# Performance work log

Measured on AMD Instinct MI355X. Metric: run time of the kernel, lower is better.

The kernel has to match this reference:

```python
import jax, jax.numpy as jnp
import numpy as np

B, N, M, C1, C2 = 8, 8192, 2048, 64, 128
MLP = [128, 128]
EPS = 1e-5


def setup_inputs() -> dict:
    key = jax.random.key(0)
    ks = jax.random.split(key, 12)
    inp = {
        'low_theta': jax.random.normal(ks[0], (B, N), jnp.float32),
        'low_phi': jax.random.normal(ks[1], (B, N), jnp.float32),
        'low_feats': jax.random.normal(ks[2], (B, C1, N), jnp.float32),
        'high_theta': jax.random.normal(ks[3], (B, M), jnp.float32),
        'high_phi': jax.random.normal(ks[4], (B, M), jnp.float32),
        'high_feats': jax.random.normal(ks[5], (B, C2, M), jnp.float32),
    }
    in_ch = C1 + C2
    # layer 0: conv1d (kernel size 1) -> weight [out, in], bias [out]; BN gamma/beta
    inp['W0'] = jax.random.normal(ks[6], (MLP[0], in_ch), jnp.float32) * 0.05
    inp['b0'] = jnp.zeros((MLP[0],), jnp.float32)
    inp['g0'] = jnp.ones((MLP[0],), jnp.float32)
    inp['beta0'] = jnp.zeros((MLP[0],), jnp.float32)
    # layer 1
    inp['W1'] = jax.random.normal(ks[7], (MLP[1], MLP[0]), jnp.float32) * 0.05
    inp['b1'] = jnp.zeros((MLP[1],), jnp.float32)
    inp['g1'] = jnp.ones((MLP[1],), jnp.float32)
    inp['beta1'] = jnp.zeros((MLP[1],), jnp.float32)
    return inp


def _conv_bn_relu(x, W, b, gamma, beta):
    # x: [B, Cin, N] -> 1x1 conv -> BN (training-mode batch stats, biased var) -> ReLU
    y = jnp.einsum('oi,bin->bon', W, x) + b[None, :, None]
    mean = jnp.mean(y, axis=(0, 2), keepdims=True)
    var = jnp.mean((y - mean) ** 2, axis=(0, 2), keepdims=True)
    yhat = (y - mean) * jax.lax.rsqrt(var + EPS)
    return jax.nn.relu(gamma[None, :, None] * yhat + beta[None, :, None])


def reference(low_theta, low_phi, low_feats, high_theta, high_phi, high_feats,
              W0, b0, g0, beta0, W1, b1, g1, beta1):
    # pairwise angular distance [B, N, M]
    dtheta = low_theta[:, :, None] - high_theta[:, None, :]
    dphi = low_phi[:, :, None] - high_phi[:, None, :]
    dist = jnp.sqrt(dtheta ** 2 + dphi ** 2)
    idx = jnp.argmin(dist, axis=-1)  # [B, N]
    # gather nearest-neighbor high features -> [B, C2, N]
    c2 = high_feats.shape[1]
    interpolated = jnp.take_along_axis(
        high_feats, jnp.broadcast_to(idx[:, None, :], (idx.shape[0], c2, idx.shape[1])), axis=2)
    cat = jnp.concatenate([low_feats, interpolated], axis=1)  # [B, C1+C2, N]
    h = _conv_bn_relu(cat, W0, b0, g0, beta0)
    out = _conv_bn_relu(h, W1, b1, g1, beta1)
    return out
```

## Files before the change

### kernel.cpp

```cpp
#include <hip/hip_runtime.h>
#include <hip/hip_bf16.h>

#define BB 8
#define NN 8192
#define MM 2048
#define C1 64
#define C2 128
#define CIN 192
#define CO 128
#define NB (BB*NN)
#define EPS 1e-5f

#define PRE_ARGMIN 2048
#define PRE_PREPH  (PRE_ARGMIN + 512)
#define PRE_TOTAL  (PRE_PREPH + 96)

typedef unsigned short u16;
typedef unsigned int u32;
typedef __bf16 bf16_t;
typedef bf16_t bf16x8 __attribute__((ext_vector_type(8)));
typedef float f32x4 __attribute__((ext_vector_type(4)));
typedef float f32x2 __attribute__((ext_vector_type(2)));

static __device__ __forceinline__ float b2f(u16 u) { return __uint_as_float(((u32)u) << 16); }
static __device__ __forceinline__ u16 f2b(float f) {
    __hip_bfloat16 h = __float2bfloat16(f);
    u16 u; __builtin_memcpy(&u, &h, 2); return u;
}

__global__ __launch_bounds__(256) void k_pre(
        const float* __restrict__ lt_, const float* __restrict__ lp_,
        const float* __restrict__ ht_, const float* __restrict__ hp_,
        const float* __restrict__ hf, const float* __restrict__ W0, const float* __restrict__ W1,
        int* __restrict__ idx, u16* __restrict__ hT,
        u16* __restrict__ W0b, u16* __restrict__ W1b) {
    __shared__ float smem[2 * 8 * 260];
    int bid = blockIdx.x, tid = threadIdx.x;

    if (bid < PRE_ARGMIN) {
        int b = bid >> 8;
        int n0 = (bid & 255) << 5;
        float* nx = smem;
        float* ny = smem + 8 * 260;
        for (int e = tid; e < MM; e += 256) {
            int p = e >> 8, i = e & 255;
            nx[p * 260 + i] = -ht_[b * MM + e];
            ny[p * 260 + i] = -hp_[b * MM + e];
        }
        __syncthreads();
        int q = tid >> 3, p = tid & 7;
        float ltv = lt_[b * NN + n0 + q];
        float lpv = lp_[b * NN + n0 + q];
        f32x2 lt2 = {ltv, ltv}, lp2 = {lpv, lpv};
        float dl[4] = {1e30f, 1e30f, 1e30f, 1e30f};
        float dpv[4] = {1e30f, 1e30f, 1e30f, 1e30f};
        int il[4] = {0, 0, 0, 0}, ipx[4] = {0, 0, 0, 0};
        const float* nxp = &nx[p * 260];
        const float* nyp = &ny[p * 260];
#pragma unroll 4
        for (int k = 0; k < 32; ++k) {
#pragma unroll
            for (int c = 0; c < 4; ++c) {
                f32x2 xx = *(const f32x2*)&nxp[(k << 3) + (c << 1)];
                f32x2 yy = *(const f32x2*)&nyp[(k << 3) + (c << 1)];
                f32x2 dt, dq, t2, u2, d2;
                asm("v_pk_add_f32 %0, %1, %2" : "=v"(dt) : "v"(lt2), "v"(xx));
                asm("v_pk_add_f32 %0, %1, %2" : "=v"(dq) : "v"(lp2), "v"(yy));
                asm("v_pk_mul_f32 %0, %1, %2" : "=v"(t2) : "v"(dt), "v"(dt));
                asm("v_pk_mul_f32 %0, %1, %2" : "=v"(u2) : "v"(dq), "v"(dq));
                asm("v_pk_add_f32 %0, %1, %2" : "=v"(d2) : "v"(t2), "v"(u2));
                int i0 = (k << 3) + (c << 1);
                bool h0 = d2[0] < dl[c];
                dpv[c] = h0 ? dl[c] : dpv[c];
                ipx[c] = h0 ? il[c] : ipx[c];
                dl[c] = h0 ? d2[0] : dl[c];
                il[c] = h0 ? i0 : il[c];
                bool h1 = d2[1] < dl[c];
                dpv[c] = h1 ? dl[c] : dpv[c];
                ipx[c] = h1 ? il[c] : ipx[c];
                dl[c] = h1 ? d2[1] : dl[c];
                il[c] = h1 ? i0 + 1 : il[c];
            }
        }
        int mbase = p << 8;
        float bs = 1e30f; int bm = 0x7fffffff;
#pragma unroll
        for (int c = 0; c < 4; ++c) {
            float sl = __fsqrt_rn(dl[c]);
            float sp = __fsqrt_rn(dpv[c]);
            int cand = mbase + ((sp == sl) ? ipx[c] : il[c]);
            if (sl < bs || (sl == bs && cand < bm)) { bs = sl; bm = cand; }
        }
#pragma unroll
        for (int d = 1; d <= 4; d <<= 1) {
            float ov = __shfl_xor(bs, d, 64);
            int om = __shfl_xor(bm, d, 64);
            if (ov < bs || (ov == bs && om < bm)) { bs = ov; bm = om; }
        }
        if (p == 0) idx[b * NN + n0 + q] = bm;
    } else if (bid < PRE_PREPH) {
        u16 (*s)[65] = (u16(*)[65])smem;
        int bid2 = bid - PRE_ARGMIN;
        int b = bid2 >> 6, m0 = ((bid2 >> 1) & 31) * 64, c0 = (bid2 & 1) * 64;
        for (int e = tid; e < 64 * 64; e += 256) {
            int i = e >> 6, j = e & 63;
            s[i][j] = f2b(hf[(b * C2 + c0 + i) * MM + m0 + j]);
        }
        __syncthreads();
        for (int e = tid; e < 64 * 64; e += 256) {
            int ii = e & 63, jj = e >> 6;
            hT[(b * MM + m0 + jj) * C2 + c0 + ii] = s[ii][jj];
        }
    } else {
        int t = (bid - PRE_PREPH) * 256 + tid;
        if (t < CIN * CO) W0b[t] = f2b(W0[t]);
        if (t < CO * CO)  W1b[t] = f2b(W1[t]);
    }
}

static __device__ __forceinline__ void epilogue(
        f32x4* ac0, f32x4* ac1, const float* bias, u16* yl,
        float* chs, float* chq, int w, int ln, int q) {
#pragma unroll
    for (int mf = 0; mf < 2; ++mf) {
        f32x4* A = mf ? ac1 : ac0;
        int chb = 32 * w + 16 * mf + 4 * q;
        float bs[4], ss[4] = {0.f, 0.f, 0.f, 0.f}, sq[4] = {0.f, 0.f, 0.f, 0.f};
#pragma unroll
        for (int r = 0; r < 4; ++r) bs[r] = bias[chb + r];
#pragma unroll
        for (int nf = 0; nf < 4; ++nf) {
            int n = (nf << 4) + ln;
#pragma unroll
            for (int r = 0; r < 4; ++r) {
                float y = A[nf][r] + bs[r];
                ss[r] += y; sq[r] += y * y;
                int o = chb + r;
                yl[(o << 6) + (n ^ ((o & 7) << 3))] = f2b(y);
            }
        }
#pragma unroll
        for (int r = 0; r < 4; ++r) {
            float v = ss[r], u2 = sq[r];
#pragma unroll
            for (int d = 1; d < 16; d <<= 1) {
                v += __shfl_xor(v, d, 64);
                u2 += __shfl_xor(u2, d, 64);
            }
            if (ln == 0) { atomicAdd(&chs[chb + r], v); atomicAdd(&chq[chb + r], u2); }
        }
    }
}

__global__ __launch_bounds__(256) void k_l0(
        const float* __restrict__ lf, const u16* __restrict__ hT, const int* __restrict__ idx,
        const u16* __restrict__ W0b, const float* __restrict__ b0,
        u16* __restrict__ y0, float* __restrict__ gpart) {
    __shared__ u16 xt[64 * CIN];
    __shared__ u16 ylds[CO * 64];
    __shared__ float chs[CO], chq[CO];
    __shared__ int idxs[64];
    int tid = threadIdx.x;
    int l = tid & 63, w = tid >> 6, ln = l & 15, q = l >> 4;
    int b = blockIdx.x >> 7, n0 = (blockIdx.x & 127) << 6;
    if (tid < 64) idxs[tid] = idx[b * NN + n0 + tid];
    if (tid < 128) { chs[tid] = 0.f; chq[tid] = 0.f; }
    __syncthreads();
    {
        const float* src = lf + (size_t)(b * C1 + l) * NN + n0 + (w << 4);
        float4 f0 = *(const float4*)src;
        float4 f1 = *(const float4*)(src + 4);
        float4 f2 = *(const float4*)(src + 8);
        float4 f3 = *(const float4*)(src + 12);
        float v[16] = {f0.x, f0.y, f0.z, f0.w, f1.x, f1.y, f1.z, f1.w,
                       f2.x, f2.y, f2.z, f2.w, f3.x, f3.y, f3.z, f3.w};
        int cc = l >> 3, clo = l & 7;
#pragma unroll
        for (int i = 0; i < 16; ++i) {
            int n = (w << 4) + i;
            xt[n * CIN + ((cc ^ (i & 7)) << 3) + clo] = f2b(v[i]);
        }
    }
    for (int e = tid; e < 1024; e += 256) {
        int n = e >> 4, c16 = e & 15;
        uint4 v = *(const uint4*)(hT + (size_t)(b * MM + idxs[n]) * C2 + (c16 << 3));
        *(uint4*)&xt[n * CIN + (((8 + c16) ^ (n & 7)) << 3)] = v;
    }
    __syncthreads();
    f32x4 ac0[4], ac1[4];
#pragma unroll
    for (int nf = 0; nf < 4; ++nf) {
        ac0[nf] = f32x4{0.f, 0.f, 0.f, 0.f};
        ac1[nf] = f32x4{0.f, 0.f, 0.f, 0.f};
    }
    const u16* w0r0 = W0b + (32 * w + ln) * CIN + 8 * q;
    const u16* w0r1 = w0r0 + 16 * CIN;
#pragma unroll
    for (int s = 0; s < 6; ++s) {
        bf16x8 a0 = *(const bf16x8*)(w0r0 + 32 * s);
        bf16x8 a1 = *(const bf16x8*)(w0r1 + 32 * s);
#pragma unroll
        for (int nf = 0; nf < 4; ++nf) {
            bf16x8 bv = *(const bf16x8*)&xt[(16 * nf + ln) * CIN + (((4 * s + q) ^ (ln & 7)) << 3)];
            ac0[nf] = __builtin_amdgcn_mfma_f32_16x16x32_bf16(a0, bv, ac0[nf], 0, 0, 0);
            ac1[nf] = __builtin_amdgcn_mfma_f32_16x16x32_bf16(a1, bv, ac1[nf], 0, 0, 0);
        }
    }
    epilogue(ac0, ac1, b0, ylds, chs, chq, w, ln, q);
    __syncthreads();
    gpart[blockIdx.x * 256 + tid] = (tid < 128) ? chs[tid] : chq[tid - 128];
    {
        int o = tid >> 1, h = tid & 1;
#pragma unroll
        for (int jj = 0; jj < 4; ++jj) {
            int j = (h << 2) + jj;
            uint4 v = *(const uint4*)&ylds[(o << 6) + ((j ^ (o & 7)) << 3)];
            *(uint4*)(y0 + (size_t)(b * CO + o) * NN + n0 + (j << 3)) = v;
        }
    }
}

__global__ __launch_bounds__(256) void k_red_scale(
        const float* __restrict__ gpart, const float* __restrict__ g,
        const float* __restrict__ be, float* __restrict__ sc, float* __restrict__ sh) {
    __shared__ float wsum[4], wsq[4];
    int o = blockIdx.x, tid = threadIdx.x;
    float s = 0.f, q = 0.f;
#pragma unroll
    for (int j = 0; j < 4; ++j) {
        int k = tid + (j << 8);
        s += gpart[k * 256 + o];
        q += gpart[k * 256 + 128 + o];
    }
#pragma unroll
    for (int d = 1; d < 64; d <<= 1) {
        s += __shfl_xor(s, d, 64);
        q += __shfl_xor(q, d, 64);
    }
    if ((tid & 63) == 0) { wsum[tid >> 6] = s; wsq[tid >> 6] = q; }
    __syncthreads();
    if (tid == 0) {
        float st = (wsum[0] + wsum[1]) + (wsum[2] + wsum[3]);
        float qt = (wsq[0] + wsq[1]) + (wsq[2] + wsq[3]);
        float mu = st * (1.f / NB);
        float var = qt * (1.f / NB) - mu * mu;
        float istd = 1.f / __fsqrt_rn(var + EPS);
        float scale = g[o] * istd;
        sc[o] = scale;
        sh[o] = be[o] - mu * scale;
    }
}

__global__ __launch_bounds__(256) void k_l1(
        u16* __restrict__ y, const float* __restrict__ sc0, const float* __restrict__ sh0,
        const u16* __restrict__ W1b, const float* __restrict__ b1,
        float* __restrict__ gpart) {
    __shared__ u16 xt[64 * CO];
    __shared__ u16 ylds[CO * 64];
    __shared__ float chs[CO], chq[CO], sc[CO], sh[CO];
    int tid = threadIdx.x;
    int l = tid & 63, w = tid >> 6, ln = l & 15, q = l >> 4;
    int b = blockIdx.x >> 7, n0 = (blockIdx.x & 127) << 6;
    if (tid < 128) {
        sc[tid] = sc0[tid]; sh[tid] = sh0[tid];
        chs[tid] = 0.f; chq[tid] = 0.f;
    }
    __syncthreads();
#pragma unroll
    for (int it = 0; it < 2; ++it) {
        int c = (it << 6) + l;
        const u16* src = y + (size_t)(b * CO + c) * NN + n0 + (w << 4);
        uint4 r0 = *(const uint4*)src;
        uint4 r1 = *(const uint4*)(src + 8);
        u16 raw[16];
        *(uint4*)&raw[0] = r0;
        *(uint4*)&raw[8] = r1;
        float scale = sc[c], shift = sh[c];
        int cc = c >> 3, clo = c & 7;
#pragma unroll
        for (int i = 0; i < 16; ++i) {
            int n = (w << 4) + i;
            float hv = fmaxf(b2f(raw[i]) * scale + shift, 0.f);
            xt[(n << 7) + ((cc ^ (i & 7)) << 3) + clo] = f2b(hv);
        }
    }
    __syncthreads();
    f32x4 ac0[4], ac1[4];
#pragma unroll
    for (int nf = 0; nf < 4; ++nf) {
        ac0[nf] = f32x4{0.f, 0.f, 0.f, 0.f};
        ac1[nf] = f32x4{0.f, 0.f, 0.f, 0.f};
    }
    const u16* w1r0 = W1b + (32 * w + ln) * CO + 8 * q;
    const u16* w1r1 = w1r0 + 16 * CO;
#pragma unroll
    for (int s = 0; s < 4; ++s) {
        bf16x8 a0 = *(const bf16x8*)(w1r0 + 32 * s);
        bf16x8 a1 = *(const bf16x8*)(w1r1 + 32 * s);
#pragma unroll
        for (int nf = 0; nf < 4; ++nf) {
            bf16x8 bv = *(const bf16x8*)&xt[((16 * nf + ln) << 7) + (((4 * s + q) ^ (ln & 7)) << 3)];
            ac0[nf] = __builtin_amdgcn_mfma_f32_16x16x32_bf16(a0, bv, ac0[nf], 0, 0, 0);
            ac1[nf] = __builtin_amdgcn_mfma_f32_16x16x32_bf16(a1, bv, ac1[nf], 0, 0, 0);
        }
    }
    epilogue(ac0, ac1, b1, ylds, chs, chq, w, ln, q);
    __syncthreads();
    gpart[blockIdx.x * 256 + tid] = (tid < 128) ? chs[tid] : chq[tid - 128];
    {
        int o = tid >> 1, h = tid & 1;
#pragma unroll
        for (int jj = 0; jj < 4; ++jj) {
            int j = (h << 2) + jj;
            uint4 v = *(const uint4*)&ylds[(o << 6) + ((j ^ (o & 7)) << 3)];
            *(uint4*)(y + (size_t)(b * CO + o) * NN + n0 + (j << 3)) = v;
        }
    }
}

__global__ __launch_bounds__(256) void k_bn1(
        const u16* __restrict__ y, const float* __restrict__ gpart,
        const float* __restrict__ g1, const float* __restrict__ be1,
        float* __restrict__ out) {
    __shared__ float wsum[4], wsq[4], bcast[2];
    int tid = threadIdx.x, bid = blockIdx.x;
    int o = (bid >> 2) & 127;
    float s = 0.f, q = 0.f;
#pragma unroll
    for (int j = 0; j < 4; ++j) {
        int k = tid + (j << 8);
        s += gpart[k * 256 + o];
        q += gpart[k * 256 + 128 + o];
    }
#pragma unroll
    for (int d = 1; d < 64; d <<= 1) {
        s += __shfl_xor(s, d, 64);
        q += __shfl_xor(q, d, 64);
    }
    if ((tid & 63) == 0) { wsum[tid >> 6] = s; wsq[tid >> 6] = q; }
    __syncthreads();
    if (tid == 0) {
        float st = (wsum[0] + wsum[1]) + (wsum[2] + wsum[3]);
        float qt = (wsq[0] + wsq[1]) + (wsq[2] + wsq[3]);
        float mu = st * (1.f / NB);
        float var = qt * (1.f / NB) - mu * mu;
        float istd = 1.f / __fsqrt_rn(var + EPS);
        float scale = g1[o] * istd;
        bcast[0] = scale;
        bcast[1] = be1[o] - mu * scale;
    }
    __syncthreads();
    float scale = bcast[0], shift = bcast[1];
    int t = bid * 256 + tid;
    size_t e0 = (size_t)t << 3;
    uint4 v = *(const uint4*)(y + e0);
    u16 raw[8];
    *(uint4*)raw = v;
    float r[8];
#pragma unroll
    for (int k = 0; k < 8; ++k)
        r[k] = fmaxf(b2f(raw[k]) * scale + shift, 0.f);
    *(float4*)(out + e0) = make_float4(r[0], r[1], r[2], r[3]);
    *(float4*)(out + e0 + 4) = make_float4(r[4], r[5], r[6], r[7]);
}

extern "C" void kernel_launch(void* const* d_in, const int* in_sizes, int n_in,
                              void* d_out, int out_size, void* d_ws, size_t ws_size,
                              hipStream_t stream) {
    const float* lt = (const float*)d_in[0];
    const float* lp = (const float*)d_in[1];
    const float* lf = (const float*)d_in[2];
    const float* ht = (const float*)d_in[3];
    const float* hp = (const float*)d_in[4];
    const float* hf = (const float*)d_in[5];
    const float* W0 = (const float*)d_in[6];
    const float* b0 = (const float*)d_in[7];
    const float* g0 = (const float*)d_in[8];
    const float* be0 = (const float*)d_in[9];
    const float* W1 = (const float*)d_in[10];
    const float* b1 = (const float*)d_in[11];
    const float* g1 = (const float*)d_in[12];
    const float* be1 = (const float*)d_in[13];

    char* ws = (char*)d_ws;
    u16* y0 = (u16*)ws;
    u16* hT = (u16*)(ws + 16777216);
    int* idx = (int*)(ws + 20971520);
    float* sc0 = (float*)(ws + 21233664);
    float* sh0 = (float*)(ws + 21234176);
    u16* W0b = (u16*)(ws + 21235712);
    u16* W1b = (u16*)(ws + 21284864);
    float* gpart = (float*)(ws + 21317632);

    k_pre<<<PRE_TOTAL, 256, 0, stream>>>(lt, lp, ht, hp, hf, W0, W1,
                                         idx, hT, W0b, W1b);
    k_l0<<<1024, 256, 0, stream>>>(lf, hT, idx, W0b, b0, y0, gpart);
    k_red_scale<<<128, 256, 0, stream>>>(gpart, g0, be0, sc0, sh0);
    k_l1<<<1024, 256, 0, stream>>>(y0, sc0, sh0, W1b, b1, gpart);
    k_bn1<<<4096, 256, 0, stream>>>(y0, gpart, g1, be1, (float*)d_out);
}
```

Before: 120.3 us.

## Read high-res coordinates as scalar operands in argmin instead of LDS staging

Result: slower. 141.7 us (+17.8%).

```diff
diff --git a/kernel.cpp b/kernel.cpp
--- a/kernel.cpp
+++ b/kernel.cpp
@@ -11,7 +11,7 @@
 #define NB (BB*NN)
 #define EPS 1e-5f
 
-#define PRE_ARGMIN 2048
+#define PRE_ARGMIN 1024
 #define PRE_PREPH  (PRE_ARGMIN + 512)
 #define PRE_TOTAL  (PRE_PREPH + 96)
 
@@ -34,42 +34,38 @@
         const float* __restrict__ hf, const float* __restrict__ W0, const float* __restrict__ W1,
         int* __restrict__ idx, u16* __restrict__ hT,
         u16* __restrict__ W0b, u16* __restrict__ W1b) {
-    __shared__ float smem[2 * 8 * 260];
+    __shared__ u16 s_t[64][65];
+    __shared__ float sm_s[256];
+    __shared__ int sm_i[256];
     int bid = blockIdx.x, tid = threadIdx.x;
 
     if (bid < PRE_ARGMIN) {
-        int b = bid >> 8;
-        int n0 = (bid & 255) << 5;
-        float* nx = smem;
-        float* ny = smem + 8 * 260;
-        for (int e = tid; e < MM; e += 256) {
-            int p = e >> 8, i = e & 255;
-            nx[p * 260 + i] = -ht_[b * MM + e];
-            ny[p * 260 + i] = -hp_[b * MM + e];
-        }
-        __syncthreads();
-        int q = tid >> 3, p = tid & 7;
-        float ltv = lt_[b * NN + n0 + q];
-        float lpv = lp_[b * NN + n0 + q];
-        f32x2 lt2 = {ltv, ltv}, lp2 = {lpv, lpv};
+        int lane = tid & 63;
+        int b = bid >> 7;
+        int n0 = (bid & 127) << 6;
+        int w = __builtin_amdgcn_readfirstlane(tid >> 6);
+        int cbase = __builtin_amdgcn_readfirstlane(b * MM + (w << 9));
+        const float* hx = ht_ + cbase;
+        const float* hy = hp_ + cbase;
+        float ltv = lt_[b * NN + n0 + lane];
+        float lpv = lp_[b * NN + n0 + lane];
+        f32x2 nlt2 = {-ltv, -ltv}, nlp2 = {-lpv, -lpv};
         float dl[4] = {1e30f, 1e30f, 1e30f, 1e30f};
         float dpv[4] = {1e30f, 1e30f, 1e30f, 1e30f};
         int il[4] = {0, 0, 0, 0}, ipx[4] = {0, 0, 0, 0};
-        const float* nxp = &nx[p * 260];
-        const float* nyp = &ny[p * 260];
 #pragma unroll 4
-        for (int k = 0; k < 32; ++k) {
+        for (int k = 0; k < 64; ++k) {
 #pragma unroll
             for (int c = 0; c < 4; ++c) {
-                f32x2 xx = *(const f32x2*)&nxp[(k << 3) + (c << 1)];
-                f32x2 yy = *(const f32x2*)&nyp[(k << 3) + (c << 1)];
+                f32x2 xx = *(const f32x2*)&hx[(c << 7) + (k << 1)];
+                f32x2 yy = *(const f32x2*)&hy[(c << 7) + (k << 1)];
                 f32x2 dt, dq, t2, u2, d2;
-                asm("v_pk_add_f32 %0, %1, %2" : "=v"(dt) : "v"(lt2), "v"(xx));
-                asm("v_pk_add_f32 %0, %1, %2" : "=v"(dq) : "v"(lp2), "v"(yy));
+                asm("v_pk_add_f32 %0, %1, %2" : "=v"(dt) : "s"(xx), "v"(nlt2));
+                asm("v_pk_add_f32 %0, %1, %2" : "=v"(dq) : "s"(yy), "v"(nlp2));
                 asm("v_pk_mul_f32 %0, %1, %2" : "=v"(t2) : "v"(dt), "v"(dt));
                 asm("v_pk_mul_f32 %0, %1, %2" : "=v"(u2) : "v"(dq), "v"(dq));
                 asm("v_pk_add_f32 %0, %1, %2" : "=v"(d2) : "v"(t2), "v"(u2));
-                int i0 = (k << 3) + (c << 1);
+                int i0 = (w << 9) + (c << 7) + (k << 1);
                 bool h0 = d2[0] < dl[c];
                 dpv[c] = h0 ? dl[c] : dpv[c];
                 ipx[c] = h0 ? il[c] : ipx[c];
@@ -82,34 +78,38 @@
                 il[c] = h1 ? i0 + 1 : il[c];
             }
         }
-        int mbase = p << 8;
         float bs = 1e30f; int bm = 0x7fffffff;
 #pragma unroll
         for (int c = 0; c < 4; ++c) {
             float sl = __fsqrt_rn(dl[c]);
             float sp = __fsqrt_rn(dpv[c]);
-            int cand = mbase + ((sp == sl) ? ipx[c] : il[c]);
+            int cand = (sp == sl) ? ipx[c] : il[c];
             if (sl < bs || (sl == bs && cand < bm)) { bs = sl; bm = cand; }
         }
-#pragma unroll
-        for (int d = 1; d <= 4; d <<= 1) {
-            float ov = __shfl_xor(bs, d, 64);
-            int om = __shfl_xor(bm, d, 64);
-            if (ov < bs || (ov == bs && om < bm)) { bs = ov; bm = om; }
-        }
-        if (p == 0) idx[b * NN + n0 + q] = bm;
+        sm_s[(w << 6) + lane] = bs;
+        sm_i[(w << 6) + lane] = bm;
+        __syncthreads();
+        if (tid < 64) {
+            float fb = sm_s[tid]; int fm = sm_i[tid];
+#pragma unroll
+            for (int w2 = 1; w2 < 4; ++w2) {
+                float ov = sm_s[(w2 << 6) + tid];
+                int om = sm_i[(w2 << 6) + tid];
+                if (ov < fb || (ov == fb && om < fm)) { fb = ov; fm = om; }
+            }
+            idx[b * NN + n0 + tid] = fm;
+        }
     } else if (bid < PRE_PREPH) {
-        u16 (*s)[65] = (u16(*)[65])smem;
         int bid2 = bid - PRE_ARGMIN;
         int b = bid2 >> 6, m0 = ((bid2 >> 1) & 31) * 64, c0 = (bid2 & 1) * 64;
         for (int e = tid; e < 64 * 64; e += 256) {
             int i = e >> 6, j = e & 63;
-            s[i][j] = f2b(hf[(b * C2 + c0 + i) * MM + m0 + j]);
+            s_t[i][j] = f2b(hf[(b * C2 + c0 + i) * MM + m0 + j]);
         }
         __syncthreads();
         for (int e = tid; e < 64 * 64; e += 256) {
             int ii = e & 63, jj = e >> 6;
-            hT[(b * MM + m0 + jj) * C2 + c0 + ii] = s[ii][jj];
+            hT[(b * MM + m0 + jj) * C2 + c0 + ii] = s_t[ii][jj];
         }
     } else {
         int t = (bid - PRE_PREPH) * 256 + tid;
```

## Fuse all stages into one persistent cooperative kernel with on-chip intermediates

Applied to the files above, without the earlier changes.

New measurement: 120.3 us. About the same (-0.0%).

```diff
diff --git a/kernel.cpp b/kernel.cpp
--- a/kernel.cpp
+++ b/kernel.cpp
@@ -1,5 +1,8 @@
 #include <hip/hip_runtime.h>
 #include <hip/hip_bf16.h>
+#include <hip/hip_cooperative_groups.h>
+
+namespace cg = cooperative_groups;
 
 #define BB 8
 #define NN 8192
@@ -11,10 +14,6 @@
 #define NB (BB*NN)
 #define EPS 1e-5f
 
-#define PRE_ARGMIN 2048
-#define PRE_PREPH  (PRE_ARGMIN + 512)
-#define PRE_TOTAL  (PRE_PREPH + 96)
-
 typedef unsigned short u16;
 typedef unsigned int u32;
 typedef __bf16 bf16_t;
@@ -27,6 +26,327 @@
     __hip_bfloat16 h = __float2bfloat16(f);
     u16 u; __builtin_memcpy(&u, &h, 2); return u;
 }
+static __device__ __forceinline__ bf16x8 cvt8(float4 x, float4 y) {
+    union { u16 u[8]; bf16x8 v; } cv;
+    cv.u[0] = f2b(x.x); cv.u[1] = f2b(x.y); cv.u[2] = f2b(x.z); cv.u[3] = f2b(x.w);
+    cv.u[4] = f2b(y.x); cv.u[5] = f2b(y.y); cv.u[6] = f2b(y.z); cv.u[7] = f2b(y.w);
+    return cv.v;
+}
+
+static __device__ __forceinline__ void epilogue(
+        f32x4* ac0, f32x4* ac1, const float* bias, u16* yl,
+        float* chs, float* chq, int w, int ln, int q) {
+#pragma unroll
+    for (int mf = 0; mf < 2; ++mf) {
+        f32x4* A = mf ? ac1 : ac0;
+        int chb = 32 * w + 16 * mf + 4 * q;
+        float bs[4], ss[4] = {0.f, 0.f, 0.f, 0.f}, sq[4] = {0.f, 0.f, 0.f, 0.f};
+#pragma unroll
+        for (int r = 0; r < 4; ++r) bs[r] = bias[chb + r];
+#pragma unroll
+        for (int nf = 0; nf < 4; ++nf) {
+            int n = (nf << 4) + ln;
+#pragma unroll
+            for (int r = 0; r < 4; ++r) {
+                float y = A[nf][r] + bs[r];
+                ss[r] += y; sq[r] += y * y;
+                int o = chb + r;
+                yl[(o << 6) + (n ^ ((o & 7) << 3))] = f2b(y);
+            }
+        }
+#pragma unroll
+        for (int r = 0; r < 4; ++r) {
+            float v = ss[r], u2 = sq[r];
+#pragma unroll
+            for (int d = 1; d < 16; d <<= 1) {
+                v += __shfl_xor(v, d, 64);
+                u2 += __shfl_xor(u2, d, 64);
+            }
+            if (ln == 0) { atomicAdd(&chs[chb + r], v); atomicAdd(&chq[chb + r], u2); }
+        }
+    }
+}
+
+struct KArgs {
+    const float *lt, *lp, *ht, *hp, *hf, *lf;
+    const float *W0, *b0, *g0, *be0, *W1, *b1, *g1, *be1;
+    float* out;
+    u16* hT;
+    float *gpart, *sc0, *sh0, *sc1, *sh1;
+};
+
+__global__ __launch_bounds__(256, 2) void k_all(KArgs a) {
+    __shared__ unsigned long long scratch8[3104];
+    __shared__ u16 ylds[2][CO * 64];
+    __shared__ float chs[CO], chq[CO], scl[CO], shl[CO];
+    __shared__ int idxs[128];
+    __shared__ float wtmp[8];
+    cg::grid_group grid = cg::this_grid();
+    int bid = blockIdx.x, tid = threadIdx.x;
+    int b = bid >> 6, blk = bid & 63;
+    int l = tid & 63, w = tid >> 6, ln = l & 15, q = l >> 4;
+
+    {
+        float* nx = (float*)scratch8;
+        float* ny = nx + 8 * 260;
+        for (int e = tid; e < MM; e += 256) {
+            int p = e >> 8, i = e & 255;
+            nx[p * 260 + i] = -a.ht[b * MM + e];
+            ny[p * 260 + i] = -a.hp[b * MM + e];
+        }
+        __syncthreads();
+        int qq = tid >> 3, p = tid & 7;
+        const float* nxp = &nx[p * 260];
+        const float* nyp = &ny[p * 260];
+        int mbase = p << 8;
+        for (int r = 0; r < 4; ++r) {
+            int n0 = blk * 128 + r * 32;
+            float ltv = a.lt[b * NN + n0 + qq], lpv = a.lp[b * NN + n0 + qq];
+            f32x2 lt2 = {ltv, ltv}, lp2 = {lpv, lpv};
+            float dl[4] = {1e30f, 1e30f, 1e30f, 1e30f};
+            float dpv[4] = {1e30f, 1e30f, 1e30f, 1e30f};
+            int il[4] = {0, 0, 0, 0}, ipx[4] = {0, 0, 0, 0};
+#pragma unroll 4
+            for (int k = 0; k < 32; ++k) {
+#pragma unroll
+                for (int c = 0; c < 4; ++c) {
+                    f32x2 xx = *(const f32x2*)&nxp[(k << 3) + (c << 1)];
+                    f32x2 yy = *(const f32x2*)&nyp[(k << 3) + (c << 1)];
+                    f32x2 dt, dp2, t2, u2, d2;
+                    asm("v_pk_add_f32 %0, %1, %2" : "=v"(dt) : "v"(lt2), "v"(xx));
+                    asm("v_pk_add_f32 %0, %1, %2" : "=v"(dp2) : "v"(lp2), "v"(yy));
+                    asm("v_pk_mul_f32 %0, %1, %2" : "=v"(t2) : "v"(dt), "v"(dt));
+                    asm("v_pk_mul_f32 %0, %1, %2" : "=v"(u2) : "v"(dp2), "v"(dp2));
+                    asm("v_pk_add_f32 %0, %1, %2" : "=v"(d2) : "v"(t2), "v"(u2));
+                    int i0 = (k << 3) + (c << 1);
+                    bool h0 = d2[0] < dl[c];
+                    dpv[c] = h0 ? dl[c] : dpv[c];
+                    ipx[c] = h0 ? il[c] : ipx[c];
+                    dl[c] = h0 ? d2[0] : dl[c];
+                    il[c] = h0 ? i0 : il[c];
+                    bool h1 = d2[1] < dl[c];
+                    dpv[c] = h1 ? dl[c] : dpv[c];
+                    ipx[c] = h1 ? il[c] : ipx[c];
+                    dl[c] = h1 ? d2[1] : dl[c];
+                    il[c] = h1 ? i0 + 1 : il[c];
+                }
+            }
+            float bs = 1e30f; int bm = 0x7fffffff;
+#pragma unroll
+            for (int c = 0; c < 4; ++c) {
+                float sl = __fsqrt_rn(dl[c]);
+                float sp = __fsqrt_rn(dpv[c]);
+                int cand = mbase + ((sp == sl) ? ipx[c] : il[c]);
+                if (sl < bs || (sl == bs && cand < bm)) { bs = sl; bm = cand; }
+            }
+#pragma unroll
+            for (int d = 1; d <= 4; d <<= 1) {
+                float ov = __shfl_xor(bs, d, 64);
+                int om = __shfl_xor(bm, d, 64);
+                if (ov < bs || (ov == bs && om < bm)) { bs = ov; bm = om; }
+            }
+            if (p == 0) idxs[r * 32 + qq] = bm;
+        }
+    }
+    __syncthreads();
+    {
+        u16 (*st)[65] = (u16(*)[65])scratch8;
+        int m0 = (blk >> 1) * 64, c0 = (blk & 1) * 64;
+        for (int e = tid; e < 4096; e += 256) {
+            int i = e >> 6, j = e & 63;
+            st[i][j] = f2b(a.hf[(b * C2 + c0 + i) * MM + m0 + j]);
+        }
+        __syncthreads();
+        for (int e = tid; e < 4096; e += 256) {
+            int ii = e & 63, jj = e >> 6;
+            a.hT[(b * MM + m0 + jj) * C2 + c0 + ii] = st[ii][jj];
+        }
+    }
+    grid.sync();
+
+    {
+        u16* xt = (u16*)scratch8;
+        if (tid < 128) { chs[tid] = 0.f; chq[tid] = 0.f; }
+        for (int tl = 0; tl < 2; ++tl) {
+            int n0 = blk * 128 + tl * 64;
+            __syncthreads();
+            {
+                const float* src = a.lf + (size_t)(b * C1 + l) * NN + n0 + (w << 4);
+                float4 f0 = *(const float4*)src;
+                float4 f1 = *(const float4*)(src + 4);
+                float4 f2 = *(const float4*)(src + 8);
+                float4 f3 = *(const float4*)(src + 12);
+                float v[16] = {f0.x, f0.y, f0.z, f0.w, f1.x, f1.y, f1.z, f1.w,
+                               f2.x, f2.y, f2.z, f2.w, f3.x, f3.y, f3.z, f3.w};
+                int cc = l >> 3, clo = l & 7;
+#pragma unroll
+                for (int i = 0; i < 16; ++i) {
+                    int n = (w << 4) + i;
+                    xt[n * CIN + ((cc ^ (i & 7)) << 3) + clo] = f2b(v[i]);
+                }
+            }
+            for (int e = tid; e < 1024; e += 256) {
+                int n = e >> 4, c16 = e & 15;
+                uint4 v = *(const uint4*)(a.hT + (size_t)(b * MM + idxs[tl * 64 + n]) * C2 + (c16 << 3));
+                *(uint4*)&xt[n * CIN + (((8 + c16) ^ (n & 7)) << 3)] = v;
+            }
+            __syncthreads();
+            f32x4 ac0[4], ac1[4];
+#pragma unroll
+            for (int nf = 0; nf < 4; ++nf) {
+                ac0[nf] = f32x4{0.f, 0.f, 0.f, 0.f};
+                ac1[nf] = f32x4{0.f, 0.f, 0.f, 0.f};
+            }
+            const float* w0r0 = a.W0 + (32 * w + ln) * CIN + 8 * q;
+            const float* w0r1 = w0r0 + 16 * CIN;
+#pragma unroll
+            for (int s = 0; s < 6; ++s) {
+                bf16x8 a0 = cvt8(*(const float4*)(w0r0 + 32 * s), *(const float4*)(w0r0 + 32 * s + 4));
+                bf16x8 a1 = cvt8(*(const float4*)(w0r1 + 32 * s), *(const float4*)(w0r1 + 32 * s + 4));
+#pragma unroll
+                for (int nf = 0; nf < 4; ++nf) {
+                    bf16x8 bv = *(const bf16x8*)&xt[(16 * nf + ln) * CIN + (((4 * s + q) ^ (ln & 7)) << 3)];
+                    ac0[nf] = __builtin_amdgcn_mfma_f32_16x16x32_bf16(a0, bv, ac0[nf], 0, 0, 0);
+                    ac1[nf] = __builtin_amdgcn_mfma_f32_16x16x32_bf16(a1, bv, ac1[nf], 0, 0, 0);
+                }
+            }
+            epilogue(ac0, ac1, a.b0, ylds[tl], chs, chq, w, ln, q);
+        }
+        __syncthreads();
+        a.gpart[bid * 256 + tid] = (tid < 128) ? chs[tid] : chq[tid - 128];
+    }
+    grid.sync();
+
+    if (bid < 128) {
+        int o = bid;
+        float s = a.gpart[tid * 256 + o] + a.gpart[(tid + 256) * 256 + o];
+        float qv = a.gpart[tid * 256 + 128 + o] + a.gpart[(tid + 256) * 256 + 128 + o];
+#pragma unroll
+        for (int d = 1; d < 64; d <<= 1) {
+            s += __shfl_xor(s, d, 64);
+            qv += __shfl_xor(qv, d, 64);
+        }
+        if ((tid & 63) == 0) { wtmp[tid >> 6] = s; wtmp[4 + (tid >> 6)] = qv; }
+        __syncthreads();
+        if (tid == 0) {
+            float st = (wtmp[0] + wtmp[1]) + (wtmp[2] + wtmp[3]);
+            float qt = (wtmp[4] + wtmp[5]) + (wtmp[6] + wtmp[7]);
+            float mu = st * (1.f / NB);
+            float var = qt * (1.f / NB) - mu * mu;
+            float istd = 1.f / __fsqrt_rn(var + EPS);
+            float scale = a.g0[o] * istd;
+            a.sc0[o] = scale;
+            a.sh0[o] = a.be0[o] - mu * scale;
+        }
+    }
+    grid.sync();
+
+    {
+        u16* xt = (u16*)scratch8;
+        if (tid < 128) {
+            scl[tid] = a.sc0[tid]; shl[tid] = a.sh0[tid];
+            chs[tid] = 0.f; chq[tid] = 0.f;
+        }
+        for (int tl = 0; tl < 2; ++tl) {
+            __syncthreads();
+#pragma unroll
+            for (int it = 0; it < 2; ++it) {
+                int c = (it << 6) + l;
+                int s5 = c & 7;
+                uint4 r0 = *(const uint4*)&ylds[tl][(c << 6) + ((((w << 1)) ^ s5) << 3)];
+                uint4 r1 = *(const uint4*)&ylds[tl][(c << 6) + ((((w << 1) + 1) ^ s5) << 3)];
+                u16 raw[16];
+                *(uint4*)&raw[0] = r0;
+                *(uint4*)&raw[8] = r1;
+                float scale = scl[c], shift = shl[c];
+                int cc = c >> 3, clo = c & 7;
+#pragma unroll
+                for (int i = 0; i < 16; ++i) {
+                    int n = (w << 4) + i;
+                    float hv = fmaxf(b2f(raw[i]) * scale + shift, 0.f);
+                    xt[(n << 7) + ((cc ^ (i & 7)) << 3) + clo] = f2b(hv);
+                }
+            }
+            __syncthreads();
+            f32x4 ac0[4], ac1[4];
+#pragma unroll
+            for (int nf = 0; nf < 4; ++nf) {
+                ac0[nf] = f32x4{0.f, 0.f, 0.f, 0.f};
+                ac1[nf] = f32x4{0.f, 0.f, 0.f, 0.f};
+            }
+            const float* w1r0 = a.W1 + (32 * w + ln) * CO + 8 * q;
+            const float* w1r1 = w1r0 + 16 * CO;
+#pragma unroll
+            for (int s = 0; s < 4; ++s) {
+                bf16x8 a0 = cvt8(*(const float4*)(w1r0 + 32 * s), *(const float4*)(w1r0 + 32 * s + 4));
+                bf16x8 a1 = cvt8(*(const float4*)(w1r1 + 32 * s), *(const float4*)(w1r1 + 32 * s + 4));
+#pragma unroll
+                for (int nf = 0; nf < 4; ++nf) {
+                    bf16x8 bv = *(const bf16x8*)&xt[((16 * nf + ln) << 7) + (((4 * s + q) ^ (ln & 7)) << 3)];
+                    ac0[nf] = __builtin_amdgcn_mfma_f32_16x16x32_bf16(a0, bv, ac0[nf], 0, 0, 0);
+                    ac1[nf] = __builtin_amdgcn_mfma_f32_16x16x32_bf16(a1, bv, ac1[nf], 0, 0, 0);
+                }
+            }
+            epilogue(ac0, ac1, a.b1, ylds[tl], chs, chq, w, ln, q);
+        }
+        __syncthreads();
+        a.gpart[bid * 256 + tid] = (tid < 128) ? chs[tid] : chq[tid - 128];
+    }
+    grid.sync();
+
+    if (bid < 128) {
+        int o = bid;
+        float s = a.gpart[tid * 256 + o] + a.gpart[(tid + 256) * 256 + o];
+        float qv = a.gpart[tid * 256 + 128 + o] + a.gpart[(tid + 256) * 256 + 128 + o];
+#pragma unroll
+        for (int d = 1; d < 64; d <<= 1) {
+            s += __shfl_xor(s, d, 64);
+            qv += __shfl_xor(qv, d, 64);
+        }
+        if ((tid & 63) == 0) { wtmp[tid >> 6] = s; wtmp[4 + (tid >> 6)] = qv; }
+        __syncthreads();
+        if (tid == 0) {
+            float st = (wtmp[0] + wtmp[1]) + (wtmp[2] + wtmp[3]);
+            float qt = (wtmp[4] + wtmp[5]) + (wtmp[6] + wtmp[7]);
+            float mu = st * (1.f / NB);
+            float var = qt * (1.f / NB) - mu * mu;
+            float istd = 1.f / __fsqrt_rn(var + EPS);
+            float scale = a.g1[o] * istd;
+            a.sc1[o] = scale;
+            a.sh1[o] = a.be1[o] - mu * scale;
+        }
+    }
+    grid.sync();
+
+    if (tid < 128) { scl[tid] = a.sc1[tid]; shl[tid] = a.sh1[tid]; }
+    __syncthreads();
+    {
+        int o = tid >> 1, h = tid & 1;
+        float scale = scl[o], shift = shl[o];
+#pragma unroll
+        for (int tl = 0; tl < 2; ++tl) {
+            int n0 = blk * 128 + tl * 64;
+#pragma unroll
+            for (int jj = 0; jj < 4; ++jj) {
+                int j = (h << 2) + jj;
+                uint4 v = *(const uint4*)&ylds[tl][(o << 6) + ((j ^ (o & 7)) << 3)];
+                u16 raw[8];
+                *(uint4*)raw = v;
+                float r[8];
+#pragma unroll
+                for (int k = 0; k < 8; ++k)
+                    r[k] = fmaxf(b2f(raw[k]) * scale + shift, 0.f);
+                float* dst = a.out + (size_t)(b * CO + o) * NN + n0 + (j << 3);
+                *(float4*)dst = make_float4(r[0], r[1], r[2], r[3]);
+                *(float4*)(dst + 4) = make_float4(r[4], r[5], r[6], r[7]);
+            }
+        }
+    }
+}
+
+#define PRE_ARGMIN 2048
+#define PRE_PREPH  (PRE_ARGMIN + 512)
+#define PRE_TOTAL  (PRE_PREPH + 96)
 
 __global__ __launch_bounds__(256) void k_pre(
         const float* __restrict__ lt_, const float* __restrict__ lp_,
@@ -36,7 +356,6 @@
         u16* __restrict__ W0b, u16* __restrict__ W1b) {
     __shared__ float smem[2 * 8 * 260];
     int bid = blockIdx.x, tid = threadIdx.x;
-
     if (bid < PRE_ARGMIN) {
         int b = bid >> 8;
         int n0 = (bid & 255) << 5;
@@ -48,9 +367,9 @@
             ny[p * 260 + i] = -hp_[b * MM + e];
         }
         __syncthreads();
-        int q = tid >> 3, p = tid & 7;
-        float ltv = lt_[b * NN + n0 + q];
-        float lpv = lp_[b * NN + n0 + q];
+        int qq = tid >> 3, p = tid & 7;
+        float ltv = lt_[b * NN + n0 + qq];
+        float lpv = lp_[b * NN + n0 + qq];
         f32x2 lt2 = {ltv, ltv}, lp2 = {lpv, lpv};
         float dl[4] = {1e30f, 1e30f, 1e30f, 1e30f};
         float dpv[4] = {1e30f, 1e30f, 1e30f, 1e30f};
@@ -63,11 +382,11 @@
             for (int c = 0; c < 4; ++c) {
                 f32x2 xx = *(const f32x2*)&nxp[(k << 3) + (c << 1)];
                 f32x2 yy = *(const f32x2*)&nyp[(k << 3) + (c << 1)];
-                f32x2 dt, dq, t2, u2, d2;
+                f32x2 dt, dp2, t2, u2, d2;
                 asm("v_pk_add_f32 %0, %1, %2" : "=v"(dt) : "v"(lt2), "v"(xx));
-                asm("v_pk_add_f32 %0, %1, %2" : "=v"(dq) : "v"(lp2), "v"(yy));
+                asm("v_pk_add_f32 %0, %1, %2" : "=v"(dp2) : "v"(lp2), "v"(yy));
                 asm("v_pk_mul_f32 %0, %1, %2" : "=v"(t2) : "v"(dt), "v"(dt));
-                asm("v_pk_mul_f32 %0, %1, %2" : "=v"(u2) : "v"(dq), "v"(dq));
+                asm("v_pk_mul_f32 %0, %1, %2" : "=v"(u2) : "v"(dp2), "v"(dp2));
                 asm("v_pk_add_f32 %0, %1, %2" : "=v"(d2) : "v"(t2), "v"(u2));
                 int i0 = (k << 3) + (c << 1);
                 bool h0 = d2[0] < dl[c];
@@ -97,7 +416,7 @@
             int om = __shfl_xor(bm, d, 64);
             if (ov < bs || (ov == bs && om < bm)) { bs = ov; bm = om; }
         }
-        if (p == 0) idx[b * NN + n0 + q] = bm;
+        if (p == 0) idx[b * NN + n0 + qq] = bm;
     } else if (bid < PRE_PREPH) {
         u16 (*s)[65] = (u16(*)[65])smem;
         int bid2 = bid - PRE_ARGMIN;
@@ -118,46 +437,12 @@
     }
 }
 
-static __device__ __forceinline__ void epilogue(
-        f32x4* ac0, f32x4* ac1, const float* bias, u16* yl,
-        float* chs, float* chq, int w, int ln, int q) {
-#pragma unroll
-    for (int mf = 0; mf < 2; ++mf) {
-        f32x4* A = mf ? ac1 : ac0;
-        int chb = 32 * w + 16 * mf + 4 * q;
-        float bs[4], ss[4] = {0.f, 0.f, 0.f, 0.f}, sq[4] = {0.f, 0.f, 0.f, 0.f};
-#pragma unroll
-        for (int r = 0; r < 4; ++r) bs[r] = bias[chb + r];
-#pragma unroll
-        for (int nf = 0; nf < 4; ++nf) {
-            int n = (nf << 4) + ln;
-#pragma unroll
-            for (int r = 0; r < 4; ++r) {
-                float y = A[nf][r] + bs[r];
-                ss[r] += y; sq[r] += y * y;
-                int o = chb + r;
-                yl[(o << 6) + (n ^ ((o & 7) << 3))] = f2b(y);
-            }
-        }
-#pragma unroll
-        for (int r = 0; r < 4; ++r) {
-            float v = ss[r], u2 = sq[r];
-#pragma unroll
-            for (int d = 1; d < 16; d <<= 1) {
-                v += __shfl_xor(v, d, 64);
-                u2 += __shfl_xor(u2, d, 64);
-            }
-            if (ln == 0) { atomicAdd(&chs[chb + r], v); atomicAdd(&chq[chb + r], u2); }
-        }
-    }
-}
-
 __global__ __launch_bounds__(256) void k_l0(
         const float* __restrict__ lf, const u16* __restrict__ hT, const int* __restrict__ idx,
         const u16* __restrict__ W0b, const float* __restrict__ b0,
         u16* __restrict__ y0, float* __restrict__ gpart) {
     __shared__ u16 xt[64 * CIN];
-    __shared__ u16 ylds[CO * 64];
+    __shared__ u16 yl[CO * 64];
     __shared__ float chs[CO], chq[CO];
     __shared__ int idxs[64];
     int tid = threadIdx.x;
@@ -206,7 +491,7 @@
             ac1[nf] = __builtin_amdgcn_mfma_f32_16x16x32_bf16(a1, bv, ac1[nf], 0, 0, 0);
         }
     }
-    epilogue(ac0, ac1, b0, ylds, chs, chq, w, ln, q);
+    epilogue(ac0, ac1, b0, yl, chs, chq, w, ln, q);
     __syncthreads();
     gpart[blockIdx.x * 256 + tid] = (tid < 128) ? chs[tid] : chq[tid - 128];
     {
@@ -214,7 +499,7 @@
 #pragma unroll
         for (int jj = 0; jj < 4; ++jj) {
             int j = (h << 2) + jj;
-            uint4 v = *(const uint4*)&ylds[(o << 6) + ((j ^ (o & 7)) << 3)];
+            uint4 v = *(const uint4*)&yl[(o << 6) + ((j ^ (o & 7)) << 3)];
             *(uint4*)(y0 + (size_t)(b * CO + o) * NN + n0 + (j << 3)) = v;
         }
     }
@@ -256,7 +541,7 @@
         const u16* __restrict__ W1b, const float* __restrict__ b1,
         float* __restrict__ gpart) {
     __shared__ u16 xt[64 * CO];
-    __shared__ u16 ylds[CO * 64];
+    __shared__ u16 yl[CO * 64];
     __shared__ float chs[CO], chq[CO], sc[CO], sh[CO];
     int tid = threadIdx.x;
     int l = tid & 63, w = tid >> 6, ln = l & 15, q = l >> 4;
@@ -304,7 +589,7 @@
             ac1[nf] = __builtin_amdgcn_mfma_f32_16x16x32_bf16(a1, bv, ac1[nf], 0, 0, 0);
         }
     }
-    epilogue(ac0, ac1, b1, ylds, chs, chq, w, ln, q);
+    epilogue(ac0, ac1, b1, yl, chs, chq, w, ln, q);
     __syncthreads();
     gpart[blockIdx.x * 256 + tid] = (tid < 128) ? chs[tid] : chq[tid - 128];
     {
@@ -312,7 +597,7 @@
 #pragma unroll
         for (int jj = 0; jj < 4; ++jj) {
             int j = (h << 2) + jj;
-            uint4 v = *(const uint4*)&ylds[(o << 6) + ((j ^ (o & 7)) << 3)];
+            uint4 v = *(const uint4*)&yl[(o << 6) + ((j ^ (o & 7)) << 3)];
             *(uint4*)(y + (size_t)(b * CO + o) * NN + n0 + (j << 3)) = v;
         }
     }
@@ -381,8 +666,24 @@
     const float* b1 = (const float*)d_in[11];
     const float* g1 = (const float*)d_in[12];
     const float* be1 = (const float*)d_in[13];
-
     char* ws = (char*)d_ws;
+
+    int maxb = 0;
+    hipError_t oerr = hipOccupancyMaxActiveBlocksPerMultiprocessor(&maxb, k_all, 256, 0);
+    if (oerr == hipSuccess && maxb >= 2) {
+        u16* hT = (u16*)ws;
+        float* gpart = (float*)(ws + 4194304);
+        float* sc0 = (float*)(ws + 4718592);
+        float* sh0 = sc0 + 128;
+        float* sc1 = sh0 + 128;
+        float* sh1 = sc1 + 128;
+        KArgs args = {lt, lp, ht, hp, hf, lf, W0, b0, g0, be0, W1, b1, g1, be1,
+                      (float*)d_out, hT, gpart, sc0, sh0, sc1, sh1};
+        void* kp[] = {&args};
+        hipError_t lerr = hipLaunchCooperativeKernel(k_all, dim3(512), dim3(256), kp, 0, stream);
+        if (lerr == hipSuccess) return;
+    }
+
     u16* y0 = (u16*)ws;
     u16* hT = (u16*)(ws + 16777216);
     int* idx = (int*)(ws + 20971520);
@@ -391,9 +692,7 @@
     u16* W0b = (u16*)(ws + 21235712);
     u16* W1b = (u16*)(ws + 21284864);
     float* gpart = (float*)(ws + 21317632);
-
-    k_pre<<<PRE_TOTAL, 256, 0, stream>>>(lt, lp, ht, hp, hf, W0, W1,
-                                         idx, hT, W0b, W1b);
+    k_pre<<<PRE_TOTAL, 256, 0, stream>>>(lt, lp, ht, hp, hf, W0, W1, idx, hT, W0b, W1b);
     k_l0<<<1024, 256, 0, stream>>>(lf, hT, idx, W0b, b0, y0, gpart);
     k_red_scale<<<128, 256, 0, stream>>>(gpart, g0, be0, sc0, sh0);
     k_l1<<<1024, 256, 0, stream>>>(y0, sc0, sh0, W1b, b1, gpart);
```
